# Kernel optimization log

Measured on AMD Instinct MI355X. Metric: run time of the kernel, lower is better.

## Reference

```python
import jax, jax.numpy as jnp
import numpy as np

N_ENT, N_REL, B, D = 100000, 500, 16, 128
P_NORM = 1
EPS = 1e-12


def _l2_normalize(x):
    # mirrors torch.nn.functional.normalize(x, 2, -1)
    n = jnp.sqrt(jnp.sum(x * x, axis=-1, keepdims=True))
    return x / jnp.maximum(n, EPS)


def setup_inputs() -> dict:
    key = jax.random.key(0)
    k0, k1, k2, k3 = jax.random.split(key, 4)
    # xavier_normal_ init: std = sqrt(2 / (fan_in + fan_out))
    ent_emb = jax.random.normal(k0, (N_ENT, D), dtype=jnp.float32) * np.sqrt(2.0 / (N_ENT + D))
    rel_emb = jax.random.normal(k1, (N_REL, D), dtype=jnp.float32) * np.sqrt(2.0 / (N_REL + D))
    e1 = jax.random.randint(k2, (B,), 0, N_ENT, dtype=jnp.int64)
    rel = jax.random.randint(k3, (B,), 0, N_REL, dtype=jnp.int64)
    X = jnp.zeros((B, D), dtype=jnp.float32)   # unused by forward (as in source)
    A = jnp.zeros((B, B), dtype=jnp.float32)   # unused by forward (as in source)
    return {"e1": e1, "rel": rel, "X": X, "A": A, "ent_emb": ent_emb, "rel_emb": rel_emb}


def reference(e1, rel, X, A, ent_emb, rel_emb) -> jnp.ndarray:
    # e1_embedded = normalize(ent_emb[e1]); rel_embedded = normalize(rel_emb[rel])
    e1_e = _l2_normalize(ent_emb[e1])          # [B, D]
    rel_e = _l2_normalize(rel_emb[rel])        # [B, D]
    node = _l2_normalize(ent_emb)              # [N, D]
    head_add_rel = e1_e + rel_e                # [B, D]
    # broadcast pairwise difference: [B, N, D]
    diff = head_add_rel[:, None, :] - node[None, :, :]
    if P_NORM == 1:
        dist = jnp.sum(jnp.abs(diff), axis=2)              # [B, N]
    else:
        dist = jnp.sum(jnp.abs(diff) ** P_NORM, axis=2) ** (1.0 / P_NORM)
    # loss_name == 'BCELoss' -> softmax over entities
    pred = jax.nn.softmax(dist, axis=-1)       # [B, N]
    return pred
```

## Files before the change

### kernel.cpp

```cpp
#include <hip/hip_runtime.h>
#include <hip/hip_bf16.h>

#define N_ENT 100000
#define NB 16
#define DIM 128
#define TILE 64
#define RSTRIDE 132
#define NBLK 1024
#define N_TILES ((N_ENT + TILE - 1) / TILE)

__global__ __launch_bounds__(128) void head_kernel(
    const int* __restrict__ e1, const int* __restrict__ rel,
    const float* __restrict__ ent, const float* __restrict__ relemb,
    float* __restrict__ head)
{
    int b = blockIdx.x, d = threadIdx.x;
    float ev = ent[e1[b] * DIM + d];
    float rv = relemb[rel[b] * DIM + d];
    __shared__ float s1[DIM], s2[DIM];
    s1[d] = ev * ev;
    s2[d] = rv * rv;
    __syncthreads();
    for (int s = 64; s > 0; s >>= 1) {
        if (d < s) { s1[d] += s1[d + s]; s2[d] += s2[d + s]; }
        __syncthreads();
    }
    float ne = fmaxf(sqrtf(s1[0]), 1e-12f);
    float nr = fmaxf(sqrtf(s2[0]), 1e-12f);
    head[b * DIM + d] = ev / ne + rv / nr;
}

__global__ __launch_bounds__(256) void dist_kernel(
    const float* __restrict__ ent, const float* __restrict__ head,
    float* __restrict__ partials, float* __restrict__ out)
{
    __shared__ float ldsRow[TILE * RSTRIDE];
    __shared__ float ldsInv[TILE];

    const int tid  = threadIdx.x;
    const int lane = tid & 63;
    const int wv   = __builtin_amdgcn_readfirstlane(tid >> 6);
    const int bbase = wv * 4;
    const float4* __restrict__ hg = (const float4*)head;

    float es0 = 0.f, es1 = 0.f, es2 = 0.f, es3 = 0.f;

    for (int tile = blockIdx.x; tile < N_TILES; tile += NBLK) {
        const int n0 = tile * TILE;
        __syncthreads();

        {
            const float4* eg = (const float4*)ent;
            #pragma unroll
            for (int i = 0; i < 8; i++) {
                int g = tid + i * 256;
                int r = g >> 5, c = g & 31;
                int gr = n0 + r;
                if (gr >= N_ENT) gr = N_ENT - 1;
                float4 v = eg[gr * (DIM / 4) + c];
                *(float4*)&ldsRow[r * RSTRIDE + c * 4] = v;
            }
        }
        __syncthreads();

        {
            int r = tid >> 2, q = tid & 3;
            const float* p = &ldsRow[r * RSTRIDE + q * 32];
            float s = 0.f;
            #pragma unroll
            for (int k = 0; k < 8; k++) {
                float4 v = *(const float4*)&p[k * 4];
                s = fmaf(v.x, v.x, s); s = fmaf(v.y, v.y, s);
                s = fmaf(v.z, v.z, s); s = fmaf(v.w, v.w, s);
            }
            s += __shfl_down(s, 2);
            s += __shfl_down(s, 1);
            if (q == 0) ldsInv[r] = 1.0f / fmaxf(sqrtf(s), 1e-12f);
        }
        __syncthreads();

        const float inv = ldsInv[lane];
        const float* rp = &ldsRow[lane * RSTRIDE];

        float a0 = 0.f, a1 = 0.f, a2 = 0.f, a3 = 0.f;
        #pragma unroll 8
        for (int j = 0; j < DIM / 4; j++) {
            float4 v  = *(const float4*)&rp[j * 4];
            float4 q0 = hg[(bbase + 0) * (DIM / 4) + j];
            float4 q1 = hg[(bbase + 1) * (DIM / 4) + j];
            float4 q2 = hg[(bbase + 2) * (DIM / 4) + j];
            float4 q3 = hg[(bbase + 3) * (DIM / 4) + j];
            a0 += fabsf(fmaf(-v.x, inv, q0.x)) + fabsf(fmaf(-v.y, inv, q0.y))
                + fabsf(fmaf(-v.z, inv, q0.z)) + fabsf(fmaf(-v.w, inv, q0.w));
            a1 += fabsf(fmaf(-v.x, inv, q1.x)) + fabsf(fmaf(-v.y, inv, q1.y))
                + fabsf(fmaf(-v.z, inv, q1.z)) + fabsf(fmaf(-v.w, inv, q1.w));
            a2 += fabsf(fmaf(-v.x, inv, q2.x)) + fabsf(fmaf(-v.y, inv, q2.y))
                + fabsf(fmaf(-v.z, inv, q2.z)) + fabsf(fmaf(-v.w, inv, q2.w));
            a3 += fabsf(fmaf(-v.x, inv, q3.x)) + fabsf(fmaf(-v.y, inv, q3.y))
                + fabsf(fmaf(-v.z, inv, q3.z)) + fabsf(fmaf(-v.w, inv, q3.w));
        }

        const int n = n0 + lane;
        const bool valid = (n < N_ENT);
        float e0 = valid ? __expf(a0) : 0.f;
        float e1 = valid ? __expf(a1) : 0.f;
        float e2 = valid ? __expf(a2) : 0.f;
        float e3 = valid ? __expf(a3) : 0.f;
        if (valid) {
            out[(bbase + 0) * N_ENT + n] = e0;
            out[(bbase + 1) * N_ENT + n] = e1;
            out[(bbase + 2) * N_ENT + n] = e2;
            out[(bbase + 3) * N_ENT + n] = e3;
        }
        es0 += e0; es1 += e1; es2 += e2; es3 += e3;
    }

#define WRED(x) { x += __shfl_down(x, 32); x += __shfl_down(x, 16); \
                  x += __shfl_down(x, 8);  x += __shfl_down(x, 4);  \
                  x += __shfl_down(x, 2);  x += __shfl_down(x, 1); }
    WRED(es0) WRED(es1) WRED(es2) WRED(es3)
#undef WRED
    if (lane == 0) {
        partials[(bbase + 0) * NBLK + blockIdx.x] = es0;
        partials[(bbase + 1) * NBLK + blockIdx.x] = es1;
        partials[(bbase + 2) * NBLK + blockIdx.x] = es2;
        partials[(bbase + 3) * NBLK + blockIdx.x] = es3;
    }
}

__global__ __launch_bounds__(256) void scale_kernel(
    float* __restrict__ out, const float* __restrict__ partials)
{
    const int b = blockIdx.y;
    const int tid = threadIdx.x;

    const int i = blockIdx.x * 256 + tid;
    float4 v = make_float4(0.f, 0.f, 0.f, 0.f);
    float4* row = (float4*)&out[b * N_ENT];
    const bool valid = (i < N_ENT / 4);
    if (valid) v = row[i];

    float s = 0.f;
    #pragma unroll
    for (int k = 0; k < NBLK / 256; k++) s += partials[b * NBLK + k * 256 + tid];
    s += __shfl_down(s, 32); s += __shfl_down(s, 16);
    s += __shfl_down(s, 8);  s += __shfl_down(s, 4);
    s += __shfl_down(s, 2);  s += __shfl_down(s, 1);
    __shared__ float red[4];
    if ((tid & 63) == 0) red[tid >> 6] = s;
    __syncthreads();
    const float invS = 1.0f / (red[0] + red[1] + red[2] + red[3]);

    if (valid) {
        v.x *= invS; v.y *= invS; v.z *= invS; v.w *= invS;
        row[i] = v;
    }
}

extern "C" void kernel_launch(void* const* d_in, const int* in_sizes, int n_in,
                              void* d_out, int out_size, void* d_ws, size_t ws_size,
                              hipStream_t stream) {
    const int*   e1     = (const int*)d_in[0];
    const int*   rel    = (const int*)d_in[1];
    const float* ent    = (const float*)d_in[4];
    const float* relemb = (const float*)d_in[5];
    float* out = (float*)d_out;

    float* head     = (float*)d_ws;
    float* partials = (float*)((char*)d_ws + 8192);

    head_kernel<<<16, 128, 0, stream>>>(e1, rel, ent, relemb, head);
    dist_kernel<<<NBLK, 256, 0, stream>>>(ent, head, partials, out);
    scale_kernel<<<dim3((N_ENT / 4 + 255) / 256, NB), 256, 0, stream>>>(out, partials);
}
```

Before: 113.3 us.

## Launch one block per entity tile with 512 threads and two queries per wave

Replaces the persistent grid-stride loop over 1024 blocks with one block per 64-entity tile (1563 blocks), each using 8 waves that handle two batch rows apiece. The scale kernel now reduces a variable number of per-tile partials. This raises parallelism and occupancy and removes the per-tile loop, but each entity tile is still loaded into LDS once per block. It adds block launch overhead and more partials to reduce.

```diff
diff --git a/kernel.cpp b/kernel.cpp
--- a/kernel.cpp
+++ b/kernel.cpp
@@ -6,7 +6,6 @@
 #define DIM 128
 #define TILE 64
 #define RSTRIDE 132
-#define NBLK 1024
 #define N_TILES ((N_ENT + TILE - 1) / TILE)
 
 __global__ __launch_bounds__(128) void head_kernel(
@@ -30,7 +29,7 @@
     head[b * DIM + d] = ev / ne + rv / nr;
 }
 
-__global__ __launch_bounds__(256) void dist_kernel(
+__global__ __launch_bounds__(512, 8) void dist_kernel(
     const float* __restrict__ ent, const float* __restrict__ head,
     float* __restrict__ partials, float* __restrict__ out)
 {
@@ -40,91 +39,73 @@
     const int tid  = threadIdx.x;
     const int lane = tid & 63;
     const int wv   = __builtin_amdgcn_readfirstlane(tid >> 6);
-    const int bbase = wv * 4;
+    const int bbase = wv * 2;
+    const int n0 = blockIdx.x * TILE;
     const float4* __restrict__ hg = (const float4*)head;
 
-    float es0 = 0.f, es1 = 0.f, es2 = 0.f, es3 = 0.f;
+    {
+        const float4* eg = (const float4*)ent;
+        #pragma unroll
+        for (int i = 0; i < 4; i++) {
+            int g = tid + i * 512;
+            int r = g >> 5, c = g & 31;
+            int gr = n0 + r;
+            if (gr >= N_ENT) gr = N_ENT - 1;
+            float4 v = eg[gr * (DIM / 4) + c];
+            *(float4*)&ldsRow[r * RSTRIDE + c * 4] = v;
+        }
+    }
+    __syncthreads();
 
-    for (int tile = blockIdx.x; tile < N_TILES; tile += NBLK) {
-        const int n0 = tile * TILE;
-        __syncthreads();
+    {
+        int r = tid >> 3, q = tid & 7;
+        const float* p = &ldsRow[r * RSTRIDE + q * 16];
+        float s = 0.f;
+        #pragma unroll
+        for (int k = 0; k < 4; k++) {
+            float4 v = *(const float4*)&p[k * 4];
+            s = fmaf(v.x, v.x, s); s = fmaf(v.y, v.y, s);
+            s = fmaf(v.z, v.z, s); s = fmaf(v.w, v.w, s);
+        }
+        s += __shfl_down(s, 4);
+        s += __shfl_down(s, 2);
+        s += __shfl_down(s, 1);
+        if (q == 0) ldsInv[r] = 1.0f / fmaxf(sqrtf(s), 1e-12f);
+    }
+    __syncthreads();
 
-        {
-            const float4* eg = (const float4*)ent;
-            #pragma unroll
-            for (int i = 0; i < 8; i++) {
-                int g = tid + i * 256;
-                int r = g >> 5, c = g & 31;
-                int gr = n0 + r;
-                if (gr >= N_ENT) gr = N_ENT - 1;
-                float4 v = eg[gr * (DIM / 4) + c];
-                *(float4*)&ldsRow[r * RSTRIDE + c * 4] = v;
-            }
-        }
-        __syncthreads();
+    const float inv = ldsInv[lane];
+    const float* rp = &ldsRow[lane * RSTRIDE];
 
-        {
-            int r = tid >> 2, q = tid & 3;
-            const float* p = &ldsRow[r * RSTRIDE + q * 32];
-            float s = 0.f;
-            #pragma unroll
-            for (int k = 0; k < 8; k++) {
-                float4 v = *(const float4*)&p[k * 4];
-                s = fmaf(v.x, v.x, s); s = fmaf(v.y, v.y, s);
-                s = fmaf(v.z, v.z, s); s = fmaf(v.w, v.w, s);
-            }
-            s += __shfl_down(s, 2);
-            s += __shfl_down(s, 1);
-            if (q == 0) ldsInv[r] = 1.0f / fmaxf(sqrtf(s), 1e-12f);
-        }
-        __syncthreads();
+    float a0 = 0.f, a1 = 0.f;
+    #pragma unroll
+    for (int j = 0; j < DIM / 4; j++) {
+        float4 v  = *(const float4*)&rp[j * 4];
+        float4 q0 = hg[(bbase + 0) * (DIM / 4) + j];
+        float4 q1 = hg[(bbase + 1) * (DIM / 4) + j];
+        a0 += fabsf(fmaf(-v.x, inv, q0.x)) + fabsf(fmaf(-v.y, inv, q0.y))
+            + fabsf(fmaf(-v.z, inv, q0.z)) + fabsf(fmaf(-v.w, inv, q0.w));
+        a1 += fabsf(fmaf(-v.x, inv, q1.x)) + fabsf(fmaf(-v.y, inv, q1.y))
+            + fabsf(fmaf(-v.z, inv, q1.z)) + fabsf(fmaf(-v.w, inv, q1.w));
+    }
 
-        const float inv = ldsInv[lane];
-        const float* rp = &ldsRow[lane * RSTRIDE];
-
-        float a0 = 0.f, a1 = 0.f, a2 = 0.f, a3 = 0.f;
-        #pragma unroll 8
-        for (int j = 0; j < DIM / 4; j++) {
-            float4 v  = *(const float4*)&rp[j * 4];
-            float4 q0 = hg[(bbase + 0) * (DIM / 4) + j];
-            float4 q1 = hg[(bbase + 1) * (DIM / 4) + j];
-            float4 q2 = hg[(bbase + 2) * (DIM / 4) + j];
-            float4 q3 = hg[(bbase + 3) * (DIM / 4) + j];
-            a0 += fabsf(fmaf(-v.x, inv, q0.x)) + fabsf(fmaf(-v.y, inv, q0.y))
-                + fabsf(fmaf(-v.z, inv, q0.z)) + fabsf(fmaf(-v.w, inv, q0.w));
-            a1 += fabsf(fmaf(-v.x, inv, q1.x)) + fabsf(fmaf(-v.y, inv, q1.y))
-                + fabsf(fmaf(-v.z, inv, q1.z)) + fabsf(fmaf(-v.w, inv, q1.w));
-            a2 += fabsf(fmaf(-v.x, inv, q2.x)) + fabsf(fmaf(-v.y, inv, q2.y))
-                + fabsf(fmaf(-v.z, inv, q2.z)) + fabsf(fmaf(-v.w, inv, q2.w));
-            a3 += fabsf(fmaf(-v.x, inv, q3.x)) + fabsf(fmaf(-v.y, inv, q3.y))
-                + fabsf(fmaf(-v.z, inv, q3.z)) + fabsf(fmaf(-v.w, inv, q3.w));
-        }
-
-        const int n = n0 + lane;
-        const bool valid = (n < N_ENT);
-        float e0 = valid ? __expf(a0) : 0.f;
-        float e1 = valid ? __expf(a1) : 0.f;
-        float e2 = valid ? __expf(a2) : 0.f;
-        float e3 = valid ? __expf(a3) : 0.f;
-        if (valid) {
-            out[(bbase + 0) * N_ENT + n] = e0;
-            out[(bbase + 1) * N_ENT + n] = e1;
-            out[(bbase + 2) * N_ENT + n] = e2;
-            out[(bbase + 3) * N_ENT + n] = e3;
-        }
-        es0 += e0; es1 += e1; es2 += e2; es3 += e3;
+    const int n = n0 + lane;
+    const bool valid = (n < N_ENT);
+    float e0 = valid ? __expf(a0) : 0.f;
+    float e1 = valid ? __expf(a1) : 0.f;
+    if (valid) {
+        out[(bbase + 0) * N_ENT + n] = e0;
+        out[(bbase + 1) * N_ENT + n] = e1;
     }
 
 #define WRED(x) { x += __shfl_down(x, 32); x += __shfl_down(x, 16); \
                   x += __shfl_down(x, 8);  x += __shfl_down(x, 4);  \
                   x += __shfl_down(x, 2);  x += __shfl_down(x, 1); }
-    WRED(es0) WRED(es1) WRED(es2) WRED(es3)
+    WRED(e0) WRED(e1)
 #undef WRED
     if (lane == 0) {
-        partials[(bbase + 0) * NBLK + blockIdx.x] = es0;
-        partials[(bbase + 1) * NBLK + blockIdx.x] = es1;
-        partials[(bbase + 2) * NBLK + blockIdx.x] = es2;
-        partials[(bbase + 3) * NBLK + blockIdx.x] = es3;
+        partials[(bbase + 0) * N_TILES + blockIdx.x] = e0;
+        partials[(bbase + 1) * N_TILES + blockIdx.x] = e1;
     }
 }
 
@@ -141,8 +122,7 @@
     if (valid) v = row[i];
 
     float s = 0.f;
-    #pragma unroll
-    for (int k = 0; k < NBLK / 256; k++) s += partials[b * NBLK + k * 256 + tid];
+    for (int k = tid; k < N_TILES; k += 256) s += partials[b * N_TILES + k];
     s += __shfl_down(s, 32); s += __shfl_down(s, 16);
     s += __shfl_down(s, 8);  s += __shfl_down(s, 4);
     s += __shfl_down(s, 2);  s += __shfl_down(s, 1);
@@ -170,6 +150,6 @@
     float* partials = (float*)((char*)d_ws + 8192);
 
     head_kernel<<<16, 128, 0, stream>>>(e1, rel, ent, relemb, head);
-    dist_kernel<<<NBLK, 256, 0, stream>>>(ent, head, partials, out);
+    dist_kernel<<<N_TILES, 512, 0, stream>>>(ent, head, partials, out);
     scale_kernel<<<dim3((N_ENT / 4 + 255) / 256, NB), 256, 0, stream>>>(out, partials);
 }
```

New measurement: 109.1 us. 3.7% less time.
